# Performance work log

Hardware: AMD Instinct MI355X
Metric: run time of the kernel (lower is better)

Reference implementation:

```python
import jax, jax.numpy as jnp
import numpy as np

THRESH = 1.0
NBITS = 3
QMAX = float(2 ** NBITS - 1)
BN_EPS = 1e-5

T, B, IN_DIM = 500, 64, 440
HID, NLAYERS, OUT = 1024, 4, 1944


def fsq(v):
    # FakeSpikeQuantization (eval): quantize membrane potential to multiples of
    # threshold, clipped to [0, 2^n_bits - 1] levels; straight-through estimator.
    q = jnp.clip(jnp.round(v / THRESH), 0.0, QMAX) * THRESH
    return v + jax.lax.stop_gradient(q - v)


def input_fsq_scan(xs):
    # vmem += x; out = fsq(vmem); vmem -= out  -- sequential over time
    def step(vmem, x):
        vmem = vmem + x
        o = fsq(vmem)
        return vmem - o, o
    _, outs = jax.lax.scan(step, jnp.zeros_like(xs[0]), xs)
    return outs


def lif_scan(ws, tau):
    # syn = w_t + tau*prev_syn; vmem += syn; out = fsq(vmem); vmem -= out
    Bb, H = ws.shape[1], ws.shape[2]
    def step(carry, w_t):
        prev_syn, vmem = carry
        syn = w_t + tau * prev_syn
        vmem = vmem + syn
        o = fsq(vmem)
        return (syn, vmem - o), o
    init = (jnp.zeros((Bb, H), ws.dtype), jnp.zeros((Bb, H), ws.dtype))
    _, outs = jax.lax.scan(step, init, ws)
    return outs


def bn_eval(x, gamma, beta):
    # BatchNorm1d in eval mode with default running stats (mean=0, var=1)
    return x / jnp.sqrt(1.0 + BN_EPS) * gamma + beta


def setup_inputs() -> dict:
    key = jax.random.key(0)
    ks = jax.random.split(key, 10)
    xs = jax.random.normal(ks[0], (T, B, IN_DIM), dtype=jnp.float32)
    # kaiming-uniform-like init scales
    W0 = jax.random.uniform(ks[1], (HID, IN_DIM), minval=-1.0, maxval=1.0) * np.sqrt(1.0 / IN_DIM)
    Ws = jax.random.uniform(ks[2], (NLAYERS - 1, HID, HID), minval=-1.0, maxval=1.0) * np.sqrt(1.0 / HID)
    taus = jnp.ones((NLAYERS, HID), dtype=jnp.float32)
    bn_gamma = jnp.ones((NLAYERS, HID), dtype=jnp.float32)
    bn_beta = jnp.zeros((NLAYERS, HID), dtype=jnp.float32)
    bound = np.sqrt(0.01 / (HID + OUT))
    Wf = jax.random.uniform(ks[3], (OUT, HID), minval=-bound, maxval=bound).astype(jnp.float32)
    fbn_gamma = jnp.ones((OUT,), dtype=jnp.float32)
    fbn_beta = jnp.zeros((OUT,), dtype=jnp.float32)
    return {"xs": xs, "W0": W0, "Ws": Ws, "taus": taus, "bn_gamma": bn_gamma,
            "bn_beta": bn_beta, "Wf": Wf, "fbn_gamma": fbn_gamma, "fbn_beta": fbn_beta}


def reference(xs, W0, Ws, taus, bn_gamma, bn_beta, Wf, fbn_gamma, fbn_beta):
    # input spike quantization
    inps = input_fsq_scan(xs)  # [T,B,IN]
    n_layers = taus.shape[0]
    for l in range(n_layers):
        W = W0 if l == 0 else Ws[l - 1]
        ws = jnp.einsum('tbi,hi->tbh', inps, W)          # dense projection (no bias; use_bn)
        ws = bn_eval(ws, bn_gamma[l], bn_beta[l])
        inps = lif_scan(ws, taus[l])                     # [T,B,H]
    logits = jnp.einsum('tbh,oh->tbo', inps, Wf)         # final linear (no bias)
    logits = bn_eval(logits, fbn_gamma, fbn_beta)
    Tt, Bb, O = logits.shape
    return jax.nn.log_softmax(logits.reshape(Tt * Bb, O), axis=1)
```

## Files before the change

### kernel.cpp

```cpp
#include <hip/hip_runtime.h>
#include <hip/hip_bf16.h>
#include <cstddef>

typedef signed char i8;
typedef unsigned int u32;
typedef int intx4 __attribute__((ext_vector_type(4)));
typedef float floatx4 __attribute__((ext_vector_type(4)));

#define T_STEPS 500
#define BATCH 64
#define INDIM 440
#define INPAD 512
#define HID 1024
#define OUTDIM 1944
#define OUTPAD 2048
#define MROWS 32000
#define INV_SQRT_BN 0.9999950000374997f
#define CH 20

__device__ __forceinline__ void g2lds16(const void* g, void* l) {
  __builtin_amdgcn_global_load_lds(
      (const __attribute__((address_space(1))) u32*)g,
      (__attribute__((address_space(3))) u32*)l, 16, 0, 0);
}

__global__ __launch_bounds__(256) void input_fsq_k(const float* __restrict__ xs,
                                                   i8* __restrict__ sp0) {
  int tid = blockIdx.x * 256 + threadIdx.x;
  int b = tid >> 9;
  int i = tid & 511;
  bool act = (i < INDIM);
  const float* src = xs + (size_t)b * INDIM + (act ? i : (INDIM - 1));
  i8* dst = sp0 + (size_t)b * INPAD + i;
  float fact = act ? 1.f : 0.f;
  const int LS = BATCH * INDIM;
  const int SS = BATCH * INPAD;
  float vmem = 0.f;
  float bufA[CH], bufB[CH];
#pragma unroll
  for (int j = 0; j < CH; ++j) bufA[j] = src[(size_t)j * LS];
  for (int it = 0; it < 12; ++it) {
    const int t0 = it * 2 * CH;
#pragma unroll
    for (int j = 0; j < CH; ++j) bufB[j] = src[(size_t)(t0 + CH + j) * LS];
#pragma unroll
    for (int j = 0; j < CH; ++j) {
      vmem += bufA[j] * fact;
      float q = fminf(fmaxf(rintf(vmem), 0.f), 7.f);
      vmem -= q;
      dst[(size_t)(t0 + j) * SS] = (i8)q;
    }
#pragma unroll
    for (int j = 0; j < CH; ++j) bufA[j] = src[(size_t)(t0 + 2 * CH + j) * LS];
#pragma unroll
    for (int j = 0; j < CH; ++j) {
      vmem += bufB[j] * fact;
      float q = fminf(fmaxf(rintf(vmem), 0.f), 7.f);
      vmem -= q;
      dst[(size_t)(t0 + CH + j) * SS] = (i8)q;
    }
  }
  const int t0 = 24 * CH;
#pragma unroll
  for (int j = 0; j < CH; ++j) {
    vmem += bufA[j] * fact;
    float q = fminf(fmaxf(rintf(vmem), 0.f), 7.f);
    vmem -= q;
    dst[(size_t)(t0 + j) * SS] = (i8)q;
  }
}

__global__ __launch_bounds__(256) void lif_k(const float* __restrict__ ws,
                                             const float* __restrict__ taus,
                                             i8* __restrict__ sp) {
  int tid = blockIdx.x * 256 + threadIdx.x;
  float tau = taus[tid & (HID - 1)];
  const float* src = ws + tid;
  i8* dst = sp + tid;
  const int S = BATCH * HID;
  float syn = 0.f, vmem = 0.f;
  float bufA[CH], bufB[CH];
#pragma unroll
  for (int j = 0; j < CH; ++j) bufA[j] = src[(size_t)j * S];
  for (int it = 0; it < 12; ++it) {
    const int t0 = it * 2 * CH;
#pragma unroll
    for (int j = 0; j < CH; ++j) bufB[j] = src[(size_t)(t0 + CH + j) * S];
#pragma unroll
    for (int j = 0; j < CH; ++j) {
      syn = fmaf(tau, syn, bufA[j]);
      vmem += syn;
      float q = fminf(fmaxf(rintf(vmem), 0.f), 7.f);
      vmem -= q;
      dst[(size_t)(t0 + j) * S] = (i8)q;
    }
#pragma unroll
    for (int j = 0; j < CH; ++j) bufA[j] = src[(size_t)(t0 + 2 * CH + j) * S];
#pragma unroll
    for (int j = 0; j < CH; ++j) {
      syn = fmaf(tau, syn, bufB[j]);
      vmem += syn;
      float q = fminf(fmaxf(rintf(vmem), 0.f), 7.f);
      vmem -= q;
      dst[(size_t)(t0 + CH + j) * S] = (i8)q;
    }
  }
  const int t0 = 24 * CH;
#pragma unroll
  for (int j = 0; j < CH; ++j) {
    syn = fmaf(tau, syn, bufA[j]);
    vmem += syn;
    float q = fminf(fmaxf(rintf(vmem), 0.f), 7.f);
    vmem -= q;
    dst[(size_t)(t0 + j) * S] = (i8)q;
  }
}

__global__ __launch_bounds__(256) void quant_rows_k(
    const float* __restrict__ W, const float* __restrict__ g,
    i8* __restrict__ Q1, i8* __restrict__ Q2,
    float* __restrict__ S1, float* __restrict__ S2,
    int K_in, int K_out, int nvalid) {
  int row = blockIdx.x * 4 + (threadIdx.x >> 6);
  int lane = threadIdx.x & 63;
  bool valid = row < nvalid;
  float gm = valid ? g[row] * INV_SQRT_BN : 0.f;
  const float* src = W + (size_t)row * K_in;
  float w[16], r[16];
  const int ne = K_out >> 6;
  float mx = 0.f;
  for (int e = 0; e < ne; ++e) {
    int k = lane + (e << 6);
    float v = (valid && k < K_in) ? src[k] * gm : 0.f;
    w[e] = v;
    mx = fmaxf(mx, fabsf(v));
  }
#pragma unroll
  for (int o = 32; o; o >>= 1) mx = fmaxf(mx, __shfl_xor(mx, o));
  float s1 = (mx > 0.f) ? mx * (1.f / 127.f) : 1.f;
  float inv1 = 1.f / s1;
  float mr = 0.f;
  for (int e = 0; e < ne; ++e) {
    float q = fminf(fmaxf(rintf(w[e] * inv1), -127.f), 127.f);
    Q1[(size_t)row * K_out + lane + (e << 6)] = (i8)q;
    float res = fmaf(-s1, q, w[e]);
    r[e] = res;
    mr = fmaxf(mr, fabsf(res));
  }
#pragma unroll
  for (int o = 32; o; o >>= 1) mr = fmaxf(mr, __shfl_xor(mr, o));
  float s2 = (mr > 0.f) ? mr * (1.f / 127.f) : 1.f;
  float inv2 = 1.f / s2;
  for (int e = 0; e < ne; ++e) {
    float q = fminf(fmaxf(rintf(r[e] * inv2), -127.f), 127.f);
    Q2[(size_t)row * K_out + lane + (e << 6)] = (i8)q;
  }
  if (lane == 0) {
    S1[row] = s1;
    S2[row] = s2;
  }
}

template <int DUAL>
__global__ __launch_bounds__(256, DUAL ? 3 : 4) void gemm_i8(
    const i8* __restrict__ A, const i8* __restrict__ B1q,
    const i8* __restrict__ B2q, const float* __restrict__ S1,
    const float* __restrict__ S2, const float* __restrict__ bias,
    float* __restrict__ C, int K, int ldc, int ncols) {
  extern __shared__ char smem[];
  char* As = smem;
  char* Bs1 = As + 128 * 128;
  char* Bs2 = DUAL ? Bs1 + 64 * 128 : Bs1;

  const int tid = threadIdx.x;
  const int m0 = blockIdx.y * 128;
  const int n0 = blockIdx.x * 64;
  const int lane = tid & 63;
  const int wave = tid >> 6;
  const int wm = (wave & 1) * 64;
  const int wn = (wave >> 1) * 32;
  const int lr = lane & 15;
  const int lq = lane >> 4;

  intx4 acc1[4][2], acc2[DUAL ? 4 : 1][2];
#pragma unroll
  for (int i = 0; i < 4; ++i)
#pragma unroll
    for (int j = 0; j < 2; ++j) {
      intx4 z = {0, 0, 0, 0};
      acc1[i][j] = z;
      if (DUAL) acc2[i][j] = z;
    }

  const int srow = tid >> 3;
  const int sj = (tid & 7) ^ (srow & 7);
  const i8* ga = A + (size_t)(m0 + srow) * K + sj * 16;
  const i8* gb1 = B1q + (size_t)(n0 + srow) * K + sj * 16;
  const i8* gb2 = DUAL ? B2q + (size_t)(n0 + srow) * K + sj * 16 : (const i8*)nullptr;
  const int ldso = tid * 16;
  const int sw = lr & 7;

  for (int k0 = 0; k0 < K; k0 += 128) {
#pragma unroll
    for (int it = 0; it < 4; ++it)
      g2lds16(ga + (size_t)(it * 32) * K + k0, As + ldso + it * 4096);
#pragma unroll
    for (int it = 0; it < 2; ++it) {
      g2lds16(gb1 + (size_t)(it * 32) * K + k0, Bs1 + ldso + it * 4096);
      if (DUAL) g2lds16(gb2 + (size_t)(it * 32) * K + k0, Bs2 + ldso + it * 4096);
    }
    __syncthreads();
#pragma unroll
    for (int kk = 0; kk < 2; ++kk) {
      const int jc = kk * 4 + lq;
      const int co = ((jc ^ sw) << 4);
      intx4 af[4];
#pragma unroll
      for (int i = 0; i < 4; ++i)
        af[i] = *(const intx4*)(As + (wm + i * 16 + lr) * 128 + co);
#pragma unroll
      for (int j = 0; j < 2; ++j) {
        const int bo = (wn + j * 16 + lr) * 128 + co;
        intx4 b1 = *(const intx4*)(Bs1 + bo);
#pragma unroll
        for (int i = 0; i < 4; ++i)
          acc1[i][j] = __builtin_amdgcn_mfma_i32_16x16x64_i8(af[i], b1, acc1[i][j], 0, 0, 0);
        if (DUAL) {
          intx4 b2 = *(const intx4*)(Bs2 + bo);
#pragma unroll
          for (int i = 0; i < 4; ++i)
            acc2[i][j] = __builtin_amdgcn_mfma_i32_16x16x64_i8(af[i], b2, acc2[i][j], 0, 0, 0);
        }
      }
    }
    __syncthreads();
  }

  float* Es = (float*)smem;
  float s1v[2], s2v[2], bv[2];
#pragma unroll
  for (int j = 0; j < 2; ++j) {
    int cg = n0 + wn + j * 16 + lr;
    s1v[j] = S1[cg];
    s2v[j] = DUAL ? S2[cg] : 0.f;
    bv[j] = (cg < ncols) ? bias[cg] : 0.f;
  }
#pragma unroll
  for (int s = 0; s < 4; ++s) {
    __syncthreads();
    if ((wave & 1) == (s >> 1)) {
#pragma unroll
      for (int ii = 0; ii < 2; ++ii) {
        int i = (s & 1) * 2 + ii;
#pragma unroll
        for (int j = 0; j < 2; ++j) {
          int cl = wn + j * 16 + lr;
#pragma unroll
          for (int r = 0; r < 4; ++r) {
            float v = fmaf(s1v[j], (float)acc1[i][j][r], bv[j]);
            if (DUAL) v = fmaf(s2v[j], (float)acc2[i][j][r], v);
            Es[(ii * 16 + lq * 4 + r) * 68 + cl] = v;
          }
        }
      }
    }
    __syncthreads();
#pragma unroll
    for (int ps = 0; ps < 2; ++ps) {
      int rl = ps * 16 + (tid >> 4);
      int c4 = (tid & 15) * 4;
      floatx4 v = *(const floatx4*)(Es + rl * 68 + c4);
      int rg = m0 + s * 32 + rl;
      int cg = n0 + c4;
      if (cg < ncols)
        *(floatx4*)(C + (size_t)rg * ldc + cg) = v;
    }
  }
}

__global__ __launch_bounds__(256) void logsoftmax_k(float* __restrict__ data) {
  __shared__ float red[8];
  float* p = data + (size_t)blockIdx.x * OUTDIM;
  const int t = threadIdx.x;
  float v[8];
  float mx = -1e30f;
#pragma unroll
  for (int j = 0; j < 8; ++j) {
    int c = t + j * 256;
    v[j] = (c < OUTDIM) ? p[c] : -1e30f;
    mx = fmaxf(mx, v[j]);
  }
#pragma unroll
  for (int o = 32; o > 0; o >>= 1) mx = fmaxf(mx, __shfl_down(mx, o));
  if ((t & 63) == 0) red[t >> 6] = mx;
  __syncthreads();
  mx = fmaxf(fmaxf(red[0], red[1]), fmaxf(red[2], red[3]));
  float s = 0.f;
#pragma unroll
  for (int j = 0; j < 8; ++j) {
    int c = t + j * 256;
    if (c < OUTDIM) s += __expf(v[j] - mx);
  }
#pragma unroll
  for (int o = 32; o > 0; o >>= 1) s += __shfl_down(s, o);
  if ((t & 63) == 0) red[4 + (t >> 6)] = s;
  __syncthreads();
  s = (red[4] + red[5]) + (red[6] + red[7]);
  float lse = mx + __logf(s);
#pragma unroll
  for (int j = 0; j < 8; ++j) {
    int c = t + j * 256;
    if (c < OUTDIM) p[c] = v[j] - lse;
  }
}

extern "C" void kernel_launch(void* const* d_in, const int* in_sizes, int n_in,
                              void* d_out, int out_size, void* d_ws, size_t ws_size,
                              hipStream_t stream) {
  const float* xs = (const float*)d_in[0];
  const float* W0 = (const float*)d_in[1];
  const float* Ws = (const float*)d_in[2];
  const float* taus = (const float*)d_in[3];
  const float* bng = (const float*)d_in[4];
  const float* bnb = (const float*)d_in[5];
  const float* Wf = (const float*)d_in[6];
  const float* fg = (const float*)d_in[7];
  const float* fb = (const float*)d_in[8];
  float* out = (float*)d_out;

  char* p = (char*)d_ws;
  i8* sp0 = (i8*)p;    p += (size_t)MROWS * INPAD;
  i8* sp = (i8*)p;     p += (size_t)MROWS * HID;
  float* wsb = (float*)p; p += (size_t)MROWS * HID * 4;
  i8* Q1_0 = (i8*)p;   p += (size_t)HID * INPAD;
  i8* Q2_0 = (i8*)p;   p += (size_t)HID * INPAD;
  i8* Q1_l = (i8*)p;   p += (size_t)3 * HID * HID;
  i8* Q2_l = (i8*)p;   p += (size_t)3 * HID * HID;
  i8* Q1_f = (i8*)p;   p += (size_t)OUTPAD * HID;
  i8* Q2_f = (i8*)p;   p += (size_t)OUTPAD * HID;
  float* S1_0 = (float*)p; p += HID * 4;
  float* S2_0 = (float*)p; p += HID * 4;
  float* S1_l = (float*)p; p += 3 * HID * 4;
  float* S2_l = (float*)p; p += 3 * HID * 4;
  float* S1_f = (float*)p; p += OUTPAD * 4;
  float* S2_f = (float*)p; p += OUTPAD * 4;

  input_fsq_k<<<(BATCH * INPAD) / 256, 256, 0, stream>>>(xs, sp0);
  quant_rows_k<<<HID / 4, 256, 0, stream>>>(W0, bng, Q1_0, Q2_0, S1_0, S2_0,
                                            INDIM, INPAD, HID);
  for (int l = 1; l < 4; ++l)
    quant_rows_k<<<HID / 4, 256, 0, stream>>>(
        Ws + (size_t)(l - 1) * HID * HID, bng + l * HID,
        Q1_l + (size_t)(l - 1) * HID * HID, Q2_l + (size_t)(l - 1) * HID * HID,
        S1_l + (l - 1) * HID, S2_l + (l - 1) * HID, HID, HID, HID);
  quant_rows_k<<<OUTPAD / 4, 256, 0, stream>>>(Wf, fg, Q1_f, Q2_f, S1_f, S2_f,
                                               HID, HID, OUTDIM);

  gemm_i8<1><<<dim3(HID / 64, MROWS / 128), 256, 32 * 1024, stream>>>(
      sp0, Q1_0, Q2_0, S1_0, S2_0, bnb, wsb, INPAD, HID, HID);
  lif_k<<<(BATCH * HID) / 256, 256, 0, stream>>>(wsb, taus, sp);
  for (int l = 1; l < 4; ++l) {
    gemm_i8<1><<<dim3(HID / 64, MROWS / 128), 256, 32 * 1024, stream>>>(
        sp, Q1_l + (size_t)(l - 1) * HID * HID, Q2_l + (size_t)(l - 1) * HID * HID,
        S1_l + (l - 1) * HID, S2_l + (l - 1) * HID, bnb + l * HID, wsb,
        HID, HID, HID);
    lif_k<<<(BATCH * HID) / 256, 256, 0, stream>>>(wsb, taus + l * HID, sp);
  }
  gemm_i8<0><<<dim3(OUTPAD / 64, MROWS / 128), 256, 24 * 1024, stream>>>(
      sp, Q1_f, (const i8*)nullptr, S1_f, (const float*)nullptr, fb, out,
      HID, OUTDIM, OUTDIM);
  logsoftmax_k<<<MROWS, 256, 0, stream>>>(out);
}
```

Baseline: 889.4 us.

## Store layer projections as 24-bit fixed point split into short and byte planes

```diff
diff --git a/kernel.cpp b/kernel.cpp
--- a/kernel.cpp
+++ b/kernel.cpp
@@ -3,9 +3,11 @@
 #include <cstddef>
 
 typedef signed char i8;
+typedef unsigned char u8;
 typedef unsigned int u32;
 typedef int intx4 __attribute__((ext_vector_type(4)));
 typedef float floatx4 __attribute__((ext_vector_type(4)));
+typedef short shortx4 __attribute__((ext_vector_type(4)));
 
 #define T_STEPS 500
 #define BATCH 64
@@ -14,9 +16,13 @@
 #define HID 1024
 #define OUTDIM 1944
 #define OUTPAD 2048
+#define NBF 31
 #define MROWS 32000
 #define INV_SQRT_BN 0.9999950000374997f
 #define CH 20
+#define WS_SCALE 524288.f
+#define WS_INV (1.f / 524288.f)
+#define WS_CLAMP 15.99994f
 
 __device__ __forceinline__ void g2lds16(const void* g, void* l) {
   __builtin_amdgcn_global_load_lds(
@@ -70,35 +76,49 @@
   }
 }
 
-__global__ __launch_bounds__(256) void lif_k(const float* __restrict__ ws,
+__global__ __launch_bounds__(256) void lif_k(const short* __restrict__ w16,
+                                             const u8* __restrict__ w8,
                                              const float* __restrict__ taus,
                                              i8* __restrict__ sp) {
   int tid = blockIdx.x * 256 + threadIdx.x;
   float tau = taus[tid & (HID - 1)];
-  const float* src = ws + tid;
+  const short* p16 = w16 + tid;
+  const u8* p8 = w8 + tid;
   i8* dst = sp + tid;
   const int S = BATCH * HID;
   float syn = 0.f, vmem = 0.f;
-  float bufA[CH], bufB[CH];
-#pragma unroll
-  for (int j = 0; j < CH; ++j) bufA[j] = src[(size_t)j * S];
+  int a16[CH], b16[CH];
+  int a8[CH], b8[CH];
+#pragma unroll
+  for (int j = 0; j < CH; ++j) {
+    a16[j] = p16[(size_t)j * S];
+    a8[j] = p8[(size_t)j * S];
+  }
   for (int it = 0; it < 12; ++it) {
     const int t0 = it * 2 * CH;
 #pragma unroll
-    for (int j = 0; j < CH; ++j) bufB[j] = src[(size_t)(t0 + CH + j) * S];
-#pragma unroll
-    for (int j = 0; j < CH; ++j) {
-      syn = fmaf(tau, syn, bufA[j]);
+    for (int j = 0; j < CH; ++j) {
+      b16[j] = p16[(size_t)(t0 + CH + j) * S];
+      b8[j] = p8[(size_t)(t0 + CH + j) * S];
+    }
+#pragma unroll
+    for (int j = 0; j < CH; ++j) {
+      float w = (float)(a16[j] * 256 + a8[j]) * WS_INV;
+      syn = fmaf(tau, syn, w);
       vmem += syn;
       float q = fminf(fmaxf(rintf(vmem), 0.f), 7.f);
       vmem -= q;
       dst[(size_t)(t0 + j) * S] = (i8)q;
     }
 #pragma unroll
-    for (int j = 0; j < CH; ++j) bufA[j] = src[(size_t)(t0 + 2 * CH + j) * S];
-#pragma unroll
-    for (int j = 0; j < CH; ++j) {
-      syn = fmaf(tau, syn, bufB[j]);
+    for (int j = 0; j < CH; ++j) {
+      a16[j] = p16[(size_t)(t0 + 2 * CH + j) * S];
+      a8[j] = p8[(size_t)(t0 + 2 * CH + j) * S];
+    }
+#pragma unroll
+    for (int j = 0; j < CH; ++j) {
+      float w = (float)(b16[j] * 256 + b8[j]) * WS_INV;
+      syn = fmaf(tau, syn, w);
       vmem += syn;
       float q = fminf(fmaxf(rintf(vmem), 0.f), 7.f);
       vmem -= q;
@@ -108,7 +128,8 @@
   const int t0 = 24 * CH;
 #pragma unroll
   for (int j = 0; j < CH; ++j) {
-    syn = fmaf(tau, syn, bufA[j]);
+    float w = (float)(a16[j] * 256 + a8[j]) * WS_INV;
+    syn = fmaf(tau, syn, w);
     vmem += syn;
     float q = fminf(fmaxf(rintf(vmem), 0.f), 7.f);
     vmem -= q;
@@ -166,7 +187,8 @@
     const i8* __restrict__ A, const i8* __restrict__ B1q,
     const i8* __restrict__ B2q, const float* __restrict__ S1,
     const float* __restrict__ S2, const float* __restrict__ bias,
-    float* __restrict__ C, int K, int ldc, int ncols) {
+    float* __restrict__ C, short* __restrict__ C16, u8* __restrict__ C8,
+    int K, int ldc, int ncols) {
   extern __shared__ char smem[];
   char* As = smem;
   char* Bs1 = As + 128 * 128;
@@ -272,8 +294,22 @@
       floatx4 v = *(const floatx4*)(Es + rl * 68 + c4);
       int rg = m0 + s * 32 + rl;
       int cg = n0 + c4;
-      if (cg < ncols)
-        *(floatx4*)(C + (size_t)rg * ldc + cg) = v;
+      if (DUAL) {
+        shortx4 hi;
+        u32 lo = 0;
+#pragma unroll
+        for (int r = 0; r < 4; ++r) {
+          float vc = fminf(WS_CLAMP, fmaxf(-WS_CLAMP, v[r]));
+          int qq = (int)rintf(vc * WS_SCALE);
+          hi[r] = (short)(qq >> 8);
+          lo |= (u32)(qq & 255) << (8 * r);
+        }
+        *(shortx4*)(C16 + (size_t)rg * ldc + cg) = hi;
+        *(u32*)(C8 + (size_t)rg * ldc + cg) = lo;
+      } else {
+        if (cg < ncols)
+          *(floatx4*)(C + (size_t)rg * ldc + cg) = v;
+      }
     }
   }
 }
@@ -331,7 +367,8 @@
   char* p = (char*)d_ws;
   i8* sp0 = (i8*)p;    p += (size_t)MROWS * INPAD;
   i8* sp = (i8*)p;     p += (size_t)MROWS * HID;
-  float* wsb = (float*)p; p += (size_t)MROWS * HID * 4;
+  short* ws16 = (short*)p; p += (size_t)MROWS * HID * 2;
+  u8* ws8 = (u8*)p;    p += (size_t)MROWS * HID;
   i8* Q1_0 = (i8*)p;   p += (size_t)HID * INPAD;
   i8* Q2_0 = (i8*)p;   p += (size_t)HID * INPAD;
   i8* Q1_l = (i8*)p;   p += (size_t)3 * HID * HID;
@@ -357,17 +394,17 @@
                                                HID, HID, OUTDIM);
 
   gemm_i8<1><<<dim3(HID / 64, MROWS / 128), 256, 32 * 1024, stream>>>(
-      sp0, Q1_0, Q2_0, S1_0, S2_0, bnb, wsb, INPAD, HID, HID);
-  lif_k<<<(BATCH * HID) / 256, 256, 0, stream>>>(wsb, taus, sp);
+      sp0, Q1_0, Q2_0, S1_0, S2_0, bnb, nullptr, ws16, ws8, INPAD, HID, HID);
+  lif_k<<<(BATCH * HID) / 256, 256, 0, stream>>>(ws16, ws8, taus, sp);
   for (int l = 1; l < 4; ++l) {
     gemm_i8<1><<<dim3(HID / 64, MROWS / 128), 256, 32 * 1024, stream>>>(
         sp, Q1_l + (size_t)(l - 1) * HID * HID, Q2_l + (size_t)(l - 1) * HID * HID,
-        S1_l + (l - 1) * HID, S2_l + (l - 1) * HID, bnb + l * HID, wsb,
-        HID, HID, HID);
-    lif_k<<<(BATCH * HID) / 256, 256, 0, stream>>>(wsb, taus + l * HID, sp);
-  }
-  gemm_i8<0><<<dim3(OUTPAD / 64, MROWS / 128), 256, 24 * 1024, stream>>>(
+        S1_l + (l - 1) * HID, S2_l + (l - 1) * HID, bnb + l * HID,
+        nullptr, ws16, ws8, HID, HID, HID);
+    lif_k<<<(BATCH * HID) / 256, 256, 0, stream>>>(ws16, ws8, taus + l * HID, sp);
+  }
+  gemm_i8<0><<<dim3(NBF, MROWS / 128), 256, 24 * 1024, stream>>>(
       sp, Q1_f, (const i8*)nullptr, S1_f, (const float*)nullptr, fb, out,
-      HID, OUTDIM, OUTDIM);
+      (short*)nullptr, (u8*)nullptr, HID, OUTDIM, OUTDIM);
   logsoftmax_k<<<MROWS, 256, 0, stream>>>(out);
 }
```

Result: no change. 897.1 us (+0.9%).
